# Performance work log

Measured on AMD Instinct MI355X. Metric: run time of the kernel, lower is better.

## Reference

```python
import jax, jax.numpy as jnp
import numpy as np

NUM_HEADS = 8
EMBED_DIM = 512
EXPAND = 3
RPE_DIM = 512
RPE_LAYERS = 3
B, N = 4, 2048
D1 = (EXPAND * EMBED_DIM) // NUM_HEADS * NUM_HEADS  # 1536
HEAD_DIM = D1 // NUM_HEADS  # 192


def srms(x):
    # SimpleRMSNorm: x / (||x||_2 * d^{-1/2} + eps)
    d = x.shape[-1]
    rms = jnp.linalg.norm(x, axis=-1, keepdims=True) * (d ** -0.5)
    return x / (rms + 1e-8)


def rpe_net(idx, Wp, bp, Wl, bl, Wr, br):
    # idx: (m, 1) relative positions -> (m, h*head_dim)
    h = idx @ Wp.T + bp
    for i in range(Wl.shape[0]):  # fixed small layer count
        h = jax.nn.relu(srms(h)) @ Wl[i].T + bl[i]
    return jax.nn.relu(srms(h)) @ Wr.T + br


def setup_inputs() -> dict:
    key = jax.random.key(0)
    ks = jax.random.split(key, 12)
    s = 0.02
    return {
        "x": jax.random.normal(ks[0], (B, N, EMBED_DIM), jnp.float32),
        "Wu": jax.random.normal(ks[1], (D1, EMBED_DIM), jnp.float32) * s,
        "bu": jnp.zeros((D1,), jnp.float32),
        "Wv": jax.random.normal(ks[2], (D1, EMBED_DIM), jnp.float32) * s,
        "bv": jnp.zeros((D1,), jnp.float32),
        "Wo": jax.random.normal(ks[3], (EMBED_DIM, D1), jnp.float32) * s,
        "bo": jnp.zeros((EMBED_DIM,), jnp.float32),
        "Wp": jax.random.normal(ks[4], (RPE_DIM, 1), jnp.float32) * s,
        "bp": jax.random.normal(ks[5], (RPE_DIM,), jnp.float32) * s,
        "Wl": jax.random.normal(ks[6], (RPE_LAYERS, RPE_DIM, RPE_DIM), jnp.float32) * s,
        "bl": jax.random.normal(ks[7], (RPE_LAYERS, RPE_DIM), jnp.float32) * s,
        "Wr": jax.random.normal(ks[8], (NUM_HEADS * HEAD_DIM, RPE_DIM), jnp.float32) * s,
        "br": jax.random.normal(ks[9], (NUM_HEADS * HEAD_DIM,), jnp.float32) * s,
    }


def reference(x, Wu, bu, Wv, bv, Wo, bo, Wp, bp, Wl, bl, Wr, br):
    b, n, e = x.shape
    d1 = Wu.shape[0]
    hd = d1 // NUM_HEADS
    u = jax.nn.silu(x @ Wu.T + bu)                       # (b, n, d1)
    v = jax.nn.silu(x @ Wv.T + bv)                       # (b, n, d1)
    v = v.reshape(b, n, NUM_HEADS, hd).transpose(0, 2, 1, 3)  # (b, h, n, d)
    # Tno non-causal, par_type=1: indices [0, 1..n-1, 0, -(n-1)..-1]
    pos = jnp.arange(1, n, dtype=x.dtype)
    zero = jnp.zeros((1,), x.dtype)
    idx = jnp.concatenate([zero, pos, zero, -pos[::-1]])[:, None]  # (2n, 1)
    a = rpe_net(idx, Wp, bp, Wl, bl, Wr, br)             # (2n, h*d)
    a = a.reshape(2 * n, NUM_HEADS, hd).transpose(1, 0, 2)  # (h, 2n, d)
    m = 2 * n
    # circular conv of length 2n along sequence, truncate to n
    y = jnp.fft.rfft(v, m, axis=2) * jnp.fft.rfft(a, m, axis=1)[None]
    out = jnp.fft.irfft(y, m, axis=2)[:, :, :n, :]       # (b, h, n, d)
    out = out.transpose(0, 2, 1, 3).reshape(b, n, d1)    # (b, n, d1)
    return (u * out) @ Wo.T + bo
```

## Files before the change

kernel.cpp:

```cpp
#include <hip/hip_runtime.h>

#define N_SEQ 2048
#define M_FFT 4096
#define D1    1536
#define NH    8
#define HD    192
#define ED    512

typedef __bf16 bf16;
typedef __bf16 bf16x4 __attribute__((ext_vector_type(4)));
typedef __bf16 bf16x8 __attribute__((ext_vector_type(8)));
typedef float  floatx4 __attribute__((ext_vector_type(4)));
typedef float  cx __attribute__((ext_vector_type(2)));

enum { MODE_PLAIN = 0, MODE_SILU_UV = 1, MODE_AT = 3, MODE_RPE = 4 };

__device__ __forceinline__ void gload16(const void* g, void* l) {
    __builtin_amdgcn_global_load_lds(
        (const __attribute__((address_space(1))) void*)g,
        (__attribute__((address_space(3))) void*)l, 16, 0, 0);
}

#define WAVE_LDS_FENCE() asm volatile("s_waitcnt lgkmcnt(0)" ::: "memory")

template<int MODE, int BN, typename OutT>
__global__ __launch_bounds__(256) void gemm_bf16(
    const bf16* __restrict__ A, const bf16* __restrict__ Bw,
    const float* __restrict__ bias, const float* __restrict__ bias2,
    OutT* __restrict__ C, OutT* __restrict__ C2,
    int M, int Nc, int K,
    const float* __restrict__ scale_in, float* __restrict__ sumsq_out)
{
    constexpr int NJ  = BN / 32;
    constexpr int ASZ = 3 * 128 * 32;
    constexpr int BSZ = 3 * BN * 32;
    __shared__ __align__(16) bf16 smem[ASZ + BSZ];
    bf16* As = smem;
    bf16* Bs = smem + ASZ;

    const int tid  = threadIdx.x;
    const int row0 = blockIdx.y * 128;
    const int col0 = blockIdx.x * BN;
    const int wid  = tid >> 6;
    const int lane = tid & 63;
    const int lm   = lane & 15;
    const int lk   = lane >> 4;
    const int wm   = wid >> 1;
    const int wn   = wid & 1;
    const int ldrow  = tid >> 2;
    const int ldcol8 = (((tid & 3) ^ ((tid >> 3) & 3))) * 8;
    const int gsw = (lk ^ ((lm >> 1) & 3)) * 8;

    floatx4 acc[4][NJ] = {};

    const bf16* Ag = A  + ((size_t)(row0 + ldrow)) * K + ldcol8;
    const bf16* Bg = Bw + ((size_t)(col0 + ldrow)) * K + ldcol8;
    const int woff = (wid * 16) * 32;

    auto stage = [&](int t, int buf) {
        const int k0 = t << 5;
        gload16(Ag + k0, &As[buf * (128 * 32) + woff]);
        gload16(Ag + (size_t)64 * K + k0, &As[buf * (128 * 32) + woff + 64 * 32]);
        gload16(Bg + k0, &Bs[buf * (BN * 32) + woff]);
        if constexpr (BN == 128)
            gload16(Bg + (size_t)64 * K + k0, &Bs[buf * (BN * 32) + woff + 64 * 32]);
    };
    auto compute = [&](int buf) {
        bf16x8 af[4], bfr[NJ];
        #pragma unroll
        for (int mi = 0; mi < 4; ++mi)
            af[mi] = *(const bf16x8*)&As[buf * (128 * 32) + (wm * 64 + mi * 16 + lm) * 32 + gsw];
        #pragma unroll
        for (int nj = 0; nj < NJ; ++nj)
            bfr[nj] = *(const bf16x8*)&Bs[buf * (BN * 32) + (wn * (BN / 2) + nj * 16 + lm) * 32 + gsw];
        __builtin_amdgcn_s_setprio(1);
        #pragma unroll
        for (int mi = 0; mi < 4; ++mi)
            #pragma unroll
            for (int nj = 0; nj < NJ; ++nj)
                acc[mi][nj] = __builtin_amdgcn_mfma_f32_16x16x32_bf16(
                    af[mi], bfr[nj], acc[mi][nj], 0, 0, 0);
        __builtin_amdgcn_s_setprio(0);
    };

    const int nt = K >> 5;
    stage(0, 0);
    stage(1, 1);
    int sb = 2, cb = 0;
    for (int t = 0; t < nt; ++t) {
        __builtin_amdgcn_s_barrier();
        __builtin_amdgcn_sched_barrier(0);
        if (t + 2 < nt) {
            stage(t + 2, sb);
            if (++sb == 3) sb = 0;
        }
        if (t < nt - 2) {
            if constexpr (BN == 128) asm volatile("s_waitcnt vmcnt(8)" ::: "memory");
            else                     asm volatile("s_waitcnt vmcnt(6)" ::: "memory");
        } else if (t == nt - 2) {
            if constexpr (BN == 128) asm volatile("s_waitcnt vmcnt(4)" ::: "memory");
            else                     asm volatile("s_waitcnt vmcnt(3)" ::: "memory");
        } else {
            asm volatile("s_waitcnt vmcnt(0)" ::: "memory");
        }
        __builtin_amdgcn_s_barrier();
        __builtin_amdgcn_sched_barrier(0);
        compute(cb);
        if (++cb == 3) cb = 0;
    }

    const float* bs = bias;
    OutT* dst = C;
    int cadj = 0;
    if (MODE == MODE_SILU_UV && col0 >= D1) { bs = bias2; dst = C2; cadj = D1; }

    float bcol[NJ];
    #pragma unroll
    for (int nj = 0; nj < NJ; ++nj)
        bcol[nj] = bs[col0 - cadj + wn * (BN / 2) + nj * 16 + lm];

    if (MODE == MODE_RPE) {
        #pragma unroll
        for (int mi = 0; mi < 4; ++mi) {
            #pragma unroll
            for (int r = 0; r < 4; ++r) {
                const int row = row0 + wm * 64 + mi * 16 + lk * 4 + r;
                float sc = 1.0f;
                if (scale_in)
                    sc = 1.0f / (sqrtf(scale_in[row]) * 0.04419417382415922f + 1e-8f);
                float ssq = 0.0f;
                #pragma unroll
                for (int nj = 0; nj < NJ; ++nj) {
                    const int col = col0 + wn * (BN / 2) + nj * 16 + lm;
                    float val = acc[mi][nj][r] * sc + bcol[nj];
                    ssq += val * val;
                    ((bf16*)C)[(size_t)row * Nc + col] = (bf16)fmaxf(val, 0.0f);
                }
                ssq += __shfl_xor(ssq, 1, 64);
                ssq += __shfl_xor(ssq, 2, 64);
                ssq += __shfl_xor(ssq, 4, 64);
                ssq += __shfl_xor(ssq, 8, 64);
                if (lm == 0) atomicAdd(&sumsq_out[row], ssq);
            }
        }
        return;
    }

    if (MODE == MODE_SILU_UV) {
        constexpr int TP = 136;
        bf16* T = smem;
        __syncthreads();
        #pragma unroll
        for (int mi = 0; mi < 4; ++mi) {
            const int rl = wm * 64 + mi * 16 + lk * 4;
            #pragma unroll
            for (int nj = 0; nj < NJ; ++nj) {
                const int cl = wn * 64 + nj * 16 + lm;
                bf16x4 o;
                #pragma unroll
                for (int r = 0; r < 4; ++r) {
                    float val = acc[mi][nj][r] + bcol[nj];
                    val = val * __fdividef(1.0f, 1.0f + __expf(-val));
                    o[r] = (bf16)val;
                }
                *(bf16x4*)&T[cl * TP + rl] = o;
            }
        }
        __syncthreads();
        const int b  = row0 >> 11;
        const int s0 = row0 & 2047;
        #pragma unroll
        for (int j = 0; j < 8; ++j) {
            const int idx = j * 256 + tid;
            const int sc  = (idx & 15) * 8;
            const int c   = idx >> 4;
            bf16x8 o = *(const bf16x8*)&T[c * TP + sc];
            *(bf16x8*)&((bf16*)dst)[((size_t)(b * D1 + col0 - cadj + c)) * N_SEQ + s0 + sc] = o;
        }
        return;
    }

    if (MODE == MODE_AT) {
        constexpr int TP = 132;
        float* Tf = (float*)smem;
        __syncthreads();
        #pragma unroll
        for (int mi = 0; mi < 4; ++mi) {
            const int rbase = row0 + wm * 64 + mi * 16 + lk * 4;
            const int rl    = wm * 64 + mi * 16 + lk * 4;
            float sc[4];
            #pragma unroll
            for (int r = 0; r < 4; ++r)
                sc[r] = scale_in
                    ? 1.0f / (sqrtf(scale_in[rbase + r]) * 0.04419417382415922f + 1e-8f)
                    : 1.0f;
            #pragma unroll
            for (int nj = 0; nj < NJ; ++nj) {
                const int cl = wn * (BN / 2) + nj * 16 + lm;
                float4 o;
                o.x = acc[mi][nj][0] * sc[0] + bcol[nj];
                o.y = acc[mi][nj][1] * sc[1] + bcol[nj];
                o.z = acc[mi][nj][2] * sc[2] + bcol[nj];
                o.w = acc[mi][nj][3] * sc[3] + bcol[nj];
                *(float4*)&Tf[cl * TP + rl] = o;
            }
        }
        __syncthreads();
        #pragma unroll
        for (int j = 0; j < 8; ++j) {
            const int idx = j * 256 + tid;
            const int rc  = (idx & 31) * 4;
            const int c   = idx >> 5;
            float4 o = *(const float4*)&Tf[c * TP + rc];
            *(float4*)&((float*)C)[(size_t)(col0 + c) * M + row0 + rc] = o;
        }
        return;
    }

    #pragma unroll
    for (int mi = 0; mi < 4; ++mi) {
        const int rbase = row0 + wm * 64 + mi * 16 + lk * 4;
        #pragma unroll
        for (int nj = 0; nj < NJ; ++nj) {
            const int col = col0 + wn * (BN / 2) + nj * 16 + lm;
            #pragma unroll
            for (int r = 0; r < 4; ++r) {
                float val = acc[mi][nj][r] + bcol[nj];
                C[(size_t)(rbase + r) * Nc + col] = (OutT)val;
            }
        }
    }
}

__global__ __launch_bounds__(256) void f2b_all_kernel(
    const float* __restrict__ x,  const float* __restrict__ s0,
    const float* __restrict__ s1, const float* __restrict__ s2,
    const float* __restrict__ s3, const float* __restrict__ s4,
    const float* __restrict__ Wp, const float* __restrict__ bp,
    bf16* __restrict__ x_bf, bf16* __restrict__ w_bf,
    float* __restrict__ sumsq, bf16* __restrict__ g0,
    float* __restrict__ twd)
{
    const int bid = blockIdx.x;
    const int tid = threadIdx.x;
    __shared__ float red[4];

    if (bid < 7936) {
        const float* src;
        bf16* dst;
        size_t off;
        if (bid < 4096) {
            src = x; dst = x_bf; off = (size_t)bid * 1024;
        } else {
            int t = bid - 4096;
            int seg = t / 768;
            src = seg == 0 ? s0 : seg == 1 ? s1 : seg == 2 ? s2
                : seg == 3 ? s3 : s4;
            dst = w_bf + (size_t)seg * 786432;
            off = (size_t)(t % 768) * 1024;
        }
        size_t i = off + (size_t)tid * 4;
        float4 f = *(const float4*)(src + i);
        union { bf16 h[4]; short4 s; } u4;
        u4.h[0] = (bf16)f.x; u4.h[1] = (bf16)f.y;
        u4.h[2] = (bf16)f.z; u4.h[3] = (bf16)f.w;
        *(short4*)(dst + i) = u4.s;
    } else if (bid < 7948) {
        size_t i = (size_t)(bid - 7936) * 1024 + (size_t)tid * 4;
        *(float4*)(sumsq + i) = make_float4(0.f, 0.f, 0.f, 0.f);
    } else if (bid < 12044) {
        const int j = bid - 7948;
        float idxv = (j < N_SEQ) ? (float)j
                                 : (j == N_SEQ ? 0.0f : (float)(j - 2 * N_SEQ));
        float h1 = idxv * Wp[tid] + bp[tid];
        float h2 = idxv * Wp[tid + 256] + bp[tid + 256];
        float ss = h1 * h1 + h2 * h2;
        #pragma unroll
        for (int off = 32; off > 0; off >>= 1) ss += __shfl_down(ss, off, 64);
        if ((tid & 63) == 0) red[tid >> 6] = ss;
        __syncthreads();
        float tot = red[0] + red[1] + red[2] + red[3];
        float scale = 1.0f / (sqrtf(tot) * 0.04419417382415922f + 1e-8f);
        g0[(size_t)j * ED + tid]       = (bf16)fmaxf(h1 * scale, 0.0f);
        g0[(size_t)j * ED + tid + 256] = (bf16)fmaxf(h2 * scale, 0.0f);
    } else {
        const int idx = (bid - 12044) * 256 + tid;
        const int j = idx >> 4, tau = idx & 15;
        float sA, cA;
        __sincosf(-6.283185307179586f * (float)(j * tau) * (1.0f / 4096.0f),
                  &sA, &cA);
        cx w; w.x = cA; w.y = sA;
        ((cx*)twd)[idx] = w;
    }
}

#define FFT_LDS_SZ 4381

__device__ __forceinline__ int fpad(int i) { return i + (i >> 4) + 2 * (i >> 8); }

__device__ __forceinline__ cx mkcx(float a, float b) { cx r; r.x = a; r.y = b; return r; }
__device__ __forceinline__ cx cmul(cx a, cx b) {
    cx br = mkcx(-b.y, b.x);
    return a.xx * b + a.yy * br;
}
__device__ __forceinline__ cx cmul_cj(cx a, cx b) {
    cx bc = mkcx(b.x, -b.y);
    cx br = mkcx(b.y, b.x);
    return a.xx * bc + a.yy * br;
}
__device__ __forceinline__ cx cneg_i(cx a) { return mkcx(a.y, -a.x); }
__device__ __forceinline__ cx cpos_i(cx a) { return mkcx(-a.y, a.x); }
__host__ __device__ constexpr int brev4(int t) {
    return ((t & 1) << 3) | ((t & 2) << 1) | ((t & 4) >> 1) | ((t & 8) >> 3);
}

#define CC1 0.9238795325112867f
#define SS1 0.3826834323650898f
#define RR2 0.7071067811865476f

template<bool HZ>
__device__ __forceinline__ void fft16_dif_r4(cx x[16]) {
    const cx W1 = mkcx( CC1, -SS1);
    const cx W2 = mkcx( RR2, -RR2);
    const cx W3 = mkcx( SS1, -CC1);
    const cx W6 = mkcx(-RR2, -RR2);
    const cx W9 = mkcx(-CC1,  SS1);
    #pragma unroll
    for (int n = 0; n < 4; ++n) {
        cx A, B, C, D;
        if (HZ) { A = x[n]; C = x[n]; B = x[n + 4]; D = x[n + 4]; }
        else {
            A = x[n] + x[n + 8];      C = x[n] - x[n + 8];
            B = x[n + 4] + x[n + 12]; D = x[n + 4] - x[n + 12];
        }
        cx s = A - B;
        cx nid = cneg_i(D);
        cx m = C + nid;
        cx p = C - nid;
        x[n] = A + B;
        if (n == 0)      { x[4] = s;            x[8]  = m;           x[12] = p; }
        else if (n == 1) { x[5] = cmul(s, W2);  x[9]  = cmul(m, W1); x[13] = cmul(p, W3); }
        else if (n == 2) { x[6] = cneg_i(s);    x[10] = cmul(m, W2); x[14] = cmul(p, W6); }
        else             { x[7] = cmul(s, W6);  x[11] = cmul(m, W3); x[15] = cmul(p, W9); }
    }
    #pragma unroll
    for (int q = 0; q < 16; q += 4) {
        cx a = x[q], b = x[q + 1], c = x[q + 2], d = x[q + 3];
        cx a1 = a + c, c1 = a - c;
        cx b1 = b + d, d1 = cneg_i(b - d);
        x[q]     = a1 + b1;
        x[q + 1] = a1 - b1;
        x[q + 2] = c1 + d1;
        x[q + 3] = c1 - d1;
    }
}

template<bool HALF_OUT>
__device__ __forceinline__ void fft16_dit_inv_r4(cx x[16]) {
    const cx V1 = mkcx( CC1, SS1);
    const cx V2 = mkcx( RR2, RR2);
    const cx V3 = mkcx( SS1, CC1);
    const cx V6 = mkcx(-RR2, RR2);
    #pragma unroll
    for (int q = 0; q < 16; q += 4) {
        cx a = x[q], b = x[q + 1], c = x[q + 2], d = x[q + 3];
        cx a1 = a + b, b1 = a - b;
        cx c1 = c + d, d1 = c - d;
        cx t = cpos_i(d1);
        x[q]     = a1 + c1;
        x[q + 2] = a1 - c1;
        x[q + 1] = b1 + t;
        x[q + 3] = b1 - t;
    }
    #pragma unroll
    for (int n = 0; n < 4; ++n) {
        cx t1, t2;
        if (n == 0)      { t1 = x[4];             t2 = x[12]; }
        else if (n == 1) { t1 = cmul(x[5],  V2);  t2 = cmul(x[13], V2); }
        else if (n == 2) { t1 = cpos_i(x[6]);     t2 = cpos_i(x[14]); }
        else             { t1 = cmul(x[7],  V6);  t2 = cmul(x[15], V6); }
        cx P = x[n] + t1, Q = x[n] - t1;
        cx R = x[n + 8] + t2, S = x[n + 8] - t2;
        cx t, u;
        if (n == 0)      { t = R;            u = S; }
        else if (n == 1) { t = cmul(R, V1);  u = cmul(S, V1); }
        else if (n == 2) { t = cmul(R, V2);  u = cmul(S, V2); }
        else             { t = cmul(R, V3);  u = cmul(S, V3); }
        cx iu = cpos_i(u);
        x[n]     = P + t;
        x[n + 4] = Q + iu;
        if (!HALF_OUT) {
            x[n + 8]  = P - t;
            x[n + 12] = Q - iu;
        }
    }
}

template<bool CONJ>
__device__ __forceinline__ void apply_tw(cx v[16], const cx tw[16]) {
    #pragma unroll
    for (int tau = 1; tau < 16; ++tau) {
        const int q = brev4(tau);
        v[q] = CONJ ? cmul_cj(v[q], tw[tau]) : cmul(v[q], tw[tau]);
    }
}

template<bool CONJ>
__device__ __forceinline__ void apply_tw_lds(cx v[16], const cx* twrow) {
    #pragma unroll
    for (int tau = 1; tau < 16; ++tau) {
        cx w = twrow[tau * 16];
        const int q = brev4(tau);
        v[q] = CONJ ? cmul_cj(v[q], w) : cmul(v[q], w);
    }
}

__device__ __forceinline__ void fwd_s1_store_hz(
    const cx vin[8], const cx tw[16], cx* d, int tid)
{
    cx x[16];
    #pragma unroll
    for (int t = 0; t < 8; ++t) x[t] = vin[t];
    fft16_dif_r4<true>(x);
    apply_tw<false>(x, tw);
    cx* base = d + fpad(tid);
    #pragma unroll
    for (int p = 0; p < 16; ++p) base[274 * p] = x[p];
}

__device__ __forceinline__ void fwd_s2(cx* d, int tid, const cx* tw2lds)
{
    cx v[16];
    cx* base = d + fpad(((tid >> 4) << 8) + (tid & 15));
    #pragma unroll
    for (int t = 0; t < 16; ++t) v[t] = base[17 * t];
    fft16_dif_r4<false>(v);
    apply_tw_lds<false>(v, tw2lds + (tid & 15));
    #pragma unroll
    for (int p = 0; p < 16; ++p) base[17 * p] = v[p];
}

__device__ __forceinline__ void fwd_s3_keep(cx* d, int tid, cx v[16])
{
    cx* base = d + fpad(tid << 4);
    #pragma unroll
    for (int t = 0; t < 16; ++t) v[t] = base[t];
    fft16_dif_r4<false>(v);
    #pragma unroll
    for (int p = 0; p < 16; ++p) base[p] = v[p];
}

__device__ __forceinline__ void inv_s2(cx* d, int tid, const cx* tw2lds)
{
    cx v[16];
    cx* base = d + fpad(((tid >> 4) << 8) + (tid & 15));
    #pragma unroll
    for (int p = 0; p < 16; ++p) v[p] = base[17 * p];
    apply_tw_lds<true>(v, tw2lds + (tid & 15));
    fft16_dit_inv_r4<false>(v);
    #pragma unroll
    for (int t = 0; t < 16; ++t) base[17 * t] = v[t];
}

__device__ __forceinline__ void inv_s3_gate(
    const cx* d, int tid, const cx tw[16],
    const bf16 ua[8], const bf16 ub[8],
    bf16* __restrict__ g0, bf16* __restrict__ g1)
{
    cx v[16];
    const cx* base = d + fpad(tid);
    #pragma unroll
    for (int p = 0; p < 16; ++p) v[p] = base[274 * p];
    apply_tw<true>(v, tw);
    fft16_dit_inv_r4<true>(v);
    #pragma unroll
    for (int t = 0; t < 8; ++t) {
        const int n = tid + 256 * t;
        g0[n] = (bf16)(v[t].x * (float)ua[t]);
        g1[n] = (bf16)(v[t].y * (float)ub[t]);
    }
}

__device__ __forceinline__ void pointwise_regs(
    const cx* d, int tid, const float4 a0pf[8], const float4 a1pf[8],
    cx v[16])
{
    auto pf = [](const float4* p, int i) -> cx {
        return (i & 1) ? mkcx(p[i >> 1].z, p[i >> 1].w)
                       : mkcx(p[i >> 1].x, p[i >> 1].y);
    };
    const int pbase = tid << 4;
    cx zm[16];
    if (tid == 0) {
        #pragma unroll
        for (int i = 0; i < 16; ++i) {
            const int p2 = (i < 2) ? i : (i ^ ((1 << (31 - __clz(i))) - 1));
            zm[i] = v[p2];
        }
    } else {
        const int mask = (1 << (31 - __clz(pbase))) - 1;
        const cx* zb2 = d + fpad((pbase ^ mask) - 15);
        #pragma unroll
        for (int i = 0; i < 16; ++i) zm[i] = zb2[15 - i];
    }
    #pragma unroll
    for (int i = 0; i < 16; ++i) {
        cx Zk = v[i];
        cx cjZm = mkcx(zm[i].x, -zm[i].y);
        cx V0 = Zk + cjZm;
        cx V1 = cneg_i(Zk - cjZm);
        v[i] = cmul(V0, pf(a0pf, i)) + cpos_i(cmul(V1, pf(a1pf, i)));
    }
}

__global__ __launch_bounds__(256, 4) void fft_a_kernel(
    const float* a_t, cx* __restrict__ A0s, cx* A1s,
    const cx* __restrict__ Twd)
{
    __shared__ cx data[FFT_LDS_SZ];
    __shared__ cx tw2lds[256];
    const int tid = threadIdx.x;
    const int r = blockIdx.x;

    cx tw[16];
    {
        const cx* Tr1 = Twd + (tid << 4);
        #pragma unroll
        for (int t = 1; t < 16; ++t) tw[t] = Tr1[t];
        tw2lds[(tid >> 4) * 16 + (tid & 15)] = Twd[(tid & 15) * 256 + (tid >> 4)];
    }

    const float* r0 = a_t + (size_t)(2 * r) * M_FFT;
    const float* r1 = r0 + M_FFT;
    cx v[16];
    #pragma unroll
    for (int t = 0; t < 16; ++t)
        v[t] = mkcx(r0[tid + 256 * t], r1[tid + 256 * t]);

    {
        fft16_dif_r4<false>(v);
        apply_tw<false>(v, tw);
        cx* base = data + fpad(tid);
        #pragma unroll
        for (int p = 0; p < 16; ++p) base[274 * p] = v[p];
    }
    __syncthreads();
    fwd_s2(data, tid, tw2lds);
    WAVE_LDS_FENCE();
    fwd_s3_keep(data, tid, v);
    __syncthreads();

    const float c = 0.25f / 4096.0f;
    const int base_i = tid << 4;
    cx* A0row = A0s + (size_t)r * 4096;
    cx* A1row = A1s + (size_t)r * 4096;
    cx wm[16];
    if (tid == 0) {
        #pragma unroll
        for (int i = 0; i < 16; ++i) {
            const int p2 = (i < 2) ? i : (i ^ ((1 << (31 - __clz(i))) - 1));
            wm[i] = v[p2];
        }
    } else {
        const int mask = (1 << (31 - __clz(base_i))) - 1;
        const cx* zb2 = data + fpad((base_i ^ mask) - 15);
        #pragma unroll
        for (int i = 0; i < 16; ++i) wm[i] = zb2[15 - i];
    }
    #pragma unroll
    for (int i = 0; i < 16; ++i) {
        cx cjWm = mkcx(wm[i].x, -wm[i].y);
        A0row[base_i + i] = c * (v[i] + cjWm);
        A1row[base_i + i] = c * cneg_i(v[i] - cjWm);
    }
}

__global__ __launch_bounds__(256, 2) void fft_conv_kernel(
    const bf16* __restrict__ v_t, const cx* __restrict__ A0s,
    const cx* __restrict__ A1s, const bf16* __restrict__ u_t,
    bf16* __restrict__ gated_t, const cx* __restrict__ Twd)
{
    __shared__ cx data[2][FFT_LDS_SZ];
    __shared__ cx tw2lds[256];
    const int tid = threadIdx.x;
    const int bx = blockIdx.x;
    const int xcd  = bx & 7;
    const int slot = bx >> 3;
    const int bp   = slot & 1;
    const int r    = (slot >> 1) * 8 + xcd;
    const int ch   = 2 * r;
    const int b0   = 2 * bp;
    const int b1   = 2 * bp + 1;

    cx tw[16];
    {
        const cx* Tr1 = Twd + (tid << 4);
        #pragma unroll
        for (int t = 1; t < 16; ++t) tw[t] = Tr1[t];
        tw2lds[(tid >> 4) * 16 + (tid & 15)] = Twd[(tid & 15) * 256 + (tid >> 4)];
    }

    const bf16* z00 = v_t + ((size_t)(b0 * D1 + ch)) * N_SEQ;
    const bf16* z01 = z00 + N_SEQ;
    const bf16* z10 = v_t + ((size_t)(b1 * D1 + ch)) * N_SEQ;
    const bf16* z11 = z10 + N_SEQ;
    {
        cx w0[8], w1[8];
        #pragma unroll
        for (int t = 0; t < 8; ++t)
            w0[t] = mkcx((float)z00[tid + 256 * t], (float)z01[tid + 256 * t]);
        #pragma unroll
        for (int t = 0; t < 8; ++t)
            w1[t] = mkcx((float)z10[tid + 256 * t], (float)z11[tid + 256 * t]);
        fwd_s1_store_hz(w0, tw, data[0], tid);
        fwd_s1_store_hz(w1, tw, data[1], tid);
    }
    __syncthreads();

    fwd_s2(data[0], tid, tw2lds);
    fwd_s2(data[1], tid, tw2lds);
    WAVE_LDS_FENCE();

    const int pbase = tid << 4;
    float4 a0pf[8], a1pf[8];
    {
        const float4* A0p = (const float4*)(A0s + (size_t)r * 4096 + pbase);
        const float4* A1p = (const float4*)(A1s + (size_t)r * 4096 + pbase);
        #pragma unroll
        for (int i = 0; i < 8; ++i) { a0pf[i] = A0p[i]; a1pf[i] = A1p[i]; }
    }
    cx vA[16], vB[16];
    fwd_s3_keep(data[0], tid, vA);
    fwd_s3_keep(data[1], tid, vB);
    __syncthreads();

    pointwise_regs(data[0], tid, a0pf, a1pf, vA);
    pointwise_regs(data[1], tid, a0pf, a1pf, vB);
    __syncthreads();
    fft16_dit_inv_r4<false>(vA);
    fft16_dit_inv_r4<false>(vB);
    {
        cx* baseA = data[0] + fpad(pbase);
        cx* baseB = data[1] + fpad(pbase);
        #pragma unroll
        for (int i = 0; i < 16; ++i) baseA[i] = vA[i];
        #pragma unroll
        for (int i = 0; i < 16; ++i) baseB[i] = vB[i];
    }
    WAVE_LDS_FENCE();

    const bf16* u00 = u_t + ((size_t)(b0 * D1 + ch)) * N_SEQ;
    const bf16* u01 = u00 + N_SEQ;
    const bf16* u10 = u_t + ((size_t)(b1 * D1 + ch)) * N_SEQ;
    const bf16* u11 = u10 + N_SEQ;
    bf16 ua0[8], ub0[8], ua1[8], ub1[8];
    #pragma unroll
    for (int t = 0; t < 8; ++t) {
        const int n = tid + 256 * t;
        ua0[t] = u00[n]; ub0[t] = u01[n];
        ua1[t] = u10[n]; ub1[t] = u11[n];
    }

    inv_s2(data[0], tid, tw2lds);
    inv_s2(data[1], tid, tw2lds);
    __syncthreads();

    bf16* g00 = gated_t + ((size_t)(b0 * D1 + ch)) * N_SEQ;
    bf16* g01 = g00 + N_SEQ;
    bf16* g10 = gated_t + ((size_t)(b1 * D1 + ch)) * N_SEQ;
    bf16* g11 = g10 + N_SEQ;
    inv_s3_gate(data[0], tid, tw, ua0, ub0, g00, g01);
    inv_s3_gate(data[1], tid, tw, ua1, ub1, g10, g11);
}

__global__ __launch_bounds__(256) void transpose_cs_kernel(
    const bf16* __restrict__ in, bf16* __restrict__ outp)
{
    __shared__ bf16 tile[64 * 68];
    const int c0 = blockIdx.x * 64;
    const int m0 = blockIdx.y * 64;
    const int b  = m0 >> 11;
    const int s0 = m0 & 2047;
    const int tid = threadIdx.x;
    const int cl = tid >> 4;
    const int sc = (tid & 15) * 4;
    #pragma unroll
    for (int p = 0; p < 4; ++p) {
        int c = p * 16 + cl;
        bf16x4 v = *(const bf16x4*)&in[((size_t)(b * D1 + c0 + c)) * N_SEQ + s0 + sc];
        *(bf16x4*)&tile[c * 68 + sc] = v;
    }
    __syncthreads();
    const int sl = tid >> 4;
    const int cc = (tid & 15) * 4;
    #pragma unroll
    for (int p = 0; p < 4; ++p) {
        int s = p * 16 + sl;
        bf16x4 o;
        #pragma unroll
        for (int j = 0; j < 4; ++j) o[j] = tile[(cc + j) * 68 + s];
        *(bf16x4*)&outp[((size_t)(m0 + s)) * D1 + c0 + cc] = o;
    }
}

extern "C" void kernel_launch(void* const* d_in, const int* in_sizes, int n_in,
                              void* d_out, int out_size, void* d_ws, size_t ws_size,
                              hipStream_t stream)
{
    const float* x  = (const float*)d_in[0];
    const float* Wu = (const float*)d_in[1];
    const float* bu = (const float*)d_in[2];
    const float* Wv = (const float*)d_in[3];
    const float* bv = (const float*)d_in[4];
    const float* Wo = (const float*)d_in[5];
    const float* bo = (const float*)d_in[6];
    const float* Wp = (const float*)d_in[7];
    const float* bp = (const float*)d_in[8];
    const float* Wl = (const float*)d_in[9];
    const float* bl = (const float*)d_in[10];
    const float* Wr = (const float*)d_in[11];
    const float* br = (const float*)d_in[12];
    float* out = (float*)d_out;

    float* ws      = (float*)d_ws;
    float* a_t     = ws;
    float* A0spec  = a_t   + 6291456;
    float* sumsq   = A0spec + 6291456;
    float* twd     = sumsq + 12288;
    bf16*  bfws    = (bf16*)(twd + 8192);
    bf16*  x_bf    = bfws;
    bf16*  w_bf    = x_bf    + 4194304;
    bf16*  Wuv_bf  = w_bf;
    bf16*  Wo_bf   = w_bf    + 2 * 786432;
    bf16*  Wl_bf   = Wo_bf   + 786432;
    bf16*  Wr_bf   = Wl_bf   + 786432;
    bf16*  gA      = Wr_bf   + 786432;
    bf16*  gB      = gA      + 2097152;
    bf16*  u_t     = gB      + 2097152;
    bf16*  v_t     = u_t     + 12582912;
    bf16*  gated_t = v_t     + 12582912;
    bf16*  gated   = gated_t + 12582912;

    dim3 blk(256);

    f2b_all_kernel<<<4096 + 5 * 768 + 12 + 4096 + 16, blk, 0, stream>>>(
        x, Wu, Wv, Wo, Wl, Wr, Wp, bp, x_bf, w_bf, sumsq, gA, twd);

    gemm_bf16<MODE_SILU_UV, 128, bf16><<<dim3(24, 64), blk, 0, stream>>>(
        x_bf, Wuv_bf, bu, bv, u_t, v_t, 8192, 2 * D1, ED, nullptr, nullptr);

    bf16* gin = gA;
    bf16* gout = gB;
    for (int i = 0; i < 3; ++i) {
        const float* sin_p = (i == 0) ? nullptr : sumsq + (size_t)(i - 1) * 4096;
        gemm_bf16<MODE_RPE, 64, bf16><<<dim3(8, 32), blk, 0, stream>>>(
            gin, Wl_bf + (size_t)i * ED * ED, bl + (size_t)i * ED, nullptr,
            gout, nullptr, 4096, ED, ED, sin_p, sumsq + (size_t)i * 4096);
        bf16* t = gin; gin = gout; gout = t;
    }
    gemm_bf16<MODE_AT, 64, float><<<dim3(24, 32), blk, 0, stream>>>(
        gin, Wr_bf, br, nullptr, a_t, nullptr, 4096, D1, ED,
        sumsq + 2 * 4096, nullptr);

    fft_a_kernel<<<768, blk, 0, stream>>>(
        a_t, (cx*)A0spec, (cx*)a_t, (const cx*)twd);
    fft_conv_kernel<<<1536, blk, 0, stream>>>(
        v_t, (const cx*)A0spec, (const cx*)a_t, u_t, gated_t, (const cx*)twd);

    transpose_cs_kernel<<<dim3(24, 128), blk, 0, stream>>>(gated_t, gated);

    gemm_bf16<MODE_PLAIN, 64, float><<<dim3(8, 64), blk, 0, stream>>>(
        gated, Wo_bf, bo, nullptr, out, nullptr, 8192, ED, D1,
        nullptr, nullptr);
}
```

Measured before the change: 315.1 us.

## Split FFT conv work across 512 threads, one batch per half-block

The FFT convolution kernel now launches 512 threads per block. Each 256-thread half handles one batch's FFT, pointwise multiply, inverse FFT and gating, where previously one thread did both batches in sequence. This doubles the threads available to hide latency and lowers per-thread register pressure, since one set of 16-element complex arrays is live instead of two. The cost is that each half loads its own copy of the A-spectrum and twiddles, and the block-wide barriers now synchronise 512 threads. The launch bounds also ask for 4 blocks per SM, which may force register spilling.

Measured after the change: 372.5 us. 1.18x slower.

```diff
diff --git a/kernel.cpp b/kernel.cpp
--- a/kernel.cpp
+++ b/kernel.cpp
@@ -575,53 +575,48 @@
     }
 }
 
-__global__ __launch_bounds__(256, 2) void fft_conv_kernel(
+__global__ __launch_bounds__(512, 4) void fft_conv_kernel(
     const bf16* __restrict__ v_t, const cx* __restrict__ A0s,
     const cx* __restrict__ A1s, const bf16* __restrict__ u_t,
     bf16* __restrict__ gated_t, const cx* __restrict__ Twd)
 {
     __shared__ cx data[2][FFT_LDS_SZ];
     __shared__ cx tw2lds[256];
-    const int tid = threadIdx.x;
+    const int tid  = threadIdx.x;
+    const int half = tid >> 8;
+    const int t2   = tid & 255;
     const int bx = blockIdx.x;
     const int xcd  = bx & 7;
     const int slot = bx >> 3;
     const int bp   = slot & 1;
     const int r    = (slot >> 1) * 8 + xcd;
     const int ch   = 2 * r;
-    const int b0   = 2 * bp;
-    const int b1   = 2 * bp + 1;
+    const int b    = 2 * bp + half;
 
     cx tw[16];
     {
-        const cx* Tr1 = Twd + (tid << 4);
+        const cx* Tr1 = Twd + (t2 << 4);
         #pragma unroll
         for (int t = 1; t < 16; ++t) tw[t] = Tr1[t];
-        tw2lds[(tid >> 4) * 16 + (tid & 15)] = Twd[(tid & 15) * 256 + (tid >> 4)];
-    }
-
-    const bf16* z00 = v_t + ((size_t)(b0 * D1 + ch)) * N_SEQ;
-    const bf16* z01 = z00 + N_SEQ;
-    const bf16* z10 = v_t + ((size_t)(b1 * D1 + ch)) * N_SEQ;
-    const bf16* z11 = z10 + N_SEQ;
+        if (tid < 256)
+            tw2lds[(t2 >> 4) * 16 + (t2 & 15)] = Twd[(t2 & 15) * 256 + (t2 >> 4)];
+    }
+
+    const bf16* z0 = v_t + ((size_t)(b * D1 + ch)) * N_SEQ;
+    const bf16* z1 = z0 + N_SEQ;
     {
-        cx w0[8], w1[8];
+        cx w0[8];
         #pragma unroll
         for (int t = 0; t < 8; ++t)
-            w0[t] = mkcx((float)z00[tid + 256 * t], (float)z01[tid + 256 * t]);
-        #pragma unroll
-        for (int t = 0; t < 8; ++t)
-            w1[t] = mkcx((float)z10[tid + 256 * t], (float)z11[tid + 256 * t]);
-        fwd_s1_store_hz(w0, tw, data[0], tid);
-        fwd_s1_store_hz(w1, tw, data[1], tid);
+            w0[t] = mkcx((float)z0[t2 + 256 * t], (float)z1[t2 + 256 * t]);
+        fwd_s1_store_hz(w0, tw, data[half], t2);
     }
     __syncthreads();
 
-    fwd_s2(data[0], tid, tw2lds);
-    fwd_s2(data[1], tid, tw2lds);
+    fwd_s2(data[half], t2, tw2lds);
     WAVE_LDS_FENCE();
 
-    const int pbase = tid << 4;
+    const int pbase = t2 << 4;
     float4 a0pf[8], a1pf[8];
     {
         const float4* A0p = (const float4*)(A0s + (size_t)r * 4096 + pbase);
@@ -629,48 +624,35 @@
         #pragma unroll
         for (int i = 0; i < 8; ++i) { a0pf[i] = A0p[i]; a1pf[i] = A1p[i]; }
     }
-    cx vA[16], vB[16];
-    fwd_s3_keep(data[0], tid, vA);
-    fwd_s3_keep(data[1], tid, vB);
+    cx v[16];
+    fwd_s3_keep(data[half], t2, v);
     __syncthreads();
 
-    pointwise_regs(data[0], tid, a0pf, a1pf, vA);
-    pointwise_regs(data[1], tid, a0pf, a1pf, vB);
+    pointwise_regs(data[half], t2, a0pf, a1pf, v);
     __syncthreads();
-    fft16_dit_inv_r4<false>(vA);
-    fft16_dit_inv_r4<false>(vB);
+    fft16_dit_inv_r4<false>(v);
     {
-        cx* baseA = data[0] + fpad(pbase);
-        cx* baseB = data[1] + fpad(pbase);
-        #pragma unroll
-        for (int i = 0; i < 16; ++i) baseA[i] = vA[i];
-        #pragma unroll
-        for (int i = 0; i < 16; ++i) baseB[i] = vB[i];
+        cx* base = data[half] + fpad(pbase);
+        #pragma unroll
+        for (int i = 0; i < 16; ++i) base[i] = v[i];
     }
     WAVE_LDS_FENCE();
 
-    const bf16* u00 = u_t + ((size_t)(b0 * D1 + ch)) * N_SEQ;
-    const bf16* u01 = u00 + N_SEQ;
-    const bf16* u10 = u_t + ((size_t)(b1 * D1 + ch)) * N_SEQ;
-    const bf16* u11 = u10 + N_SEQ;
-    bf16 ua0[8], ub0[8], ua1[8], ub1[8];
+    const bf16* u0 = u_t + ((size_t)(b * D1 + ch)) * N_SEQ;
+    const bf16* u1 = u0 + N_SEQ;
+    bf16 ua[8], ub[8];
     #pragma unroll
     for (int t = 0; t < 8; ++t) {
-        const int n = tid + 256 * t;
-        ua0[t] = u00[n]; ub0[t] = u01[n];
-        ua1[t] = u10[n]; ub1[t] = u11[n];
-    }
-
-    inv_s2(data[0], tid, tw2lds);
-    inv_s2(data[1], tid, tw2lds);
+        const int n = t2 + 256 * t;
+        ua[t] = u0[n]; ub[t] = u1[n];
+    }
+
+    inv_s2(data[half], t2, tw2lds);
     __syncthreads();
 
-    bf16* g00 = gated_t + ((size_t)(b0 * D1 + ch)) * N_SEQ;
-    bf16* g01 = g00 + N_SEQ;
-    bf16* g10 = gated_t + ((size_t)(b1 * D1 + ch)) * N_SEQ;
-    bf16* g11 = g10 + N_SEQ;
-    inv_s3_gate(data[0], tid, tw, ua0, ub0, g00, g01);
-    inv_s3_gate(data[1], tid, tw, ua1, ub1, g10, g11);
+    bf16* g0 = gated_t + ((size_t)(b * D1 + ch)) * N_SEQ;
+    bf16* g1 = g0 + N_SEQ;
+    inv_s3_gate(data[half], t2, tw, ua, ub, g0, g1);
 }
 
 __global__ __launch_bounds__(256) void transpose_cs_kernel(
@@ -764,7 +746,7 @@
 
     fft_a_kernel<<<768, blk, 0, stream>>>(
         a_t, (cx*)A0spec, (cx*)a_t, (const cx*)twd);
-    fft_conv_kernel<<<1536, blk, 0, stream>>>(
+    fft_conv_kernel<<<1536, dim3(512), 0, stream>>>(
         v_t, (const cx*)A0spec, (const cx*)a_t, u_t, gated_t, (const cx*)twd);
 
     transpose_cs_kernel<<<dim3(24, 128), blk, 0, stream>>>(gated_t, gated);
```
